# Kernel tuning notes

Measured on AMD Instinct MI355X. Metric: run time of the kernel, lower is better.

Reference implementation:

```python
import jax, jax.numpy as jnp
import numpy as np

N_NODES = 50000
N_EDGES = 800000
D_IN = 64
D_HID = 64
D_OUT = 64


def setup_inputs() -> dict:
    key = jax.random.key(0)
    ks = jax.random.split(key, 10)
    x = jax.random.normal(ks[0], (N_NODES, D_IN), dtype=jnp.float32)
    src = jax.random.randint(ks[1], (N_EDGES,), 0, N_NODES, dtype=jnp.int32)
    dst = jax.random.randint(ks[2], (N_EDGES,), 0, N_NODES, dtype=jnp.int32)
    s = 1.0 / np.sqrt(D_IN)
    W0 = jax.random.uniform(ks[3], (D_IN, D_HID), jnp.float32, -s, s)
    b0 = jnp.zeros((D_HID,), jnp.float32)
    W1 = jax.random.uniform(ks[4], (D_HID, D_HID), jnp.float32, -s, s)
    b1 = jnp.zeros((D_HID,), jnp.float32)
    W2 = jax.random.uniform(ks[5], (D_HID, D_OUT), jnp.float32, -s, s)
    b2 = jnp.zeros((D_OUT,), jnp.float32)
    return {"x": x, "src": src, "dst": dst, "W0": W0, "b0": b0,
            "W1": W1, "b1": b1, "W2": W2, "b2": b2}


def reference(x, src, dst, W0, b0, W1, b1, W2, b2):
    N = x.shape[0]
    # in-degree (constant across layers)
    deg = jax.ops.segment_sum(jnp.ones(src.shape[0], x.dtype), dst, num_segments=N)
    inv = (1.0 / (deg + 1.0))[:, None]  # [N,1] gcn normalizer (deg + self)

    def sage_gcn(h, W, b):
        # gather neighbor feats along edges, scatter-add to destinations
        agg = jax.ops.segment_sum(h[src], dst, num_segments=N)  # [N,d]
        h_neigh = (agg + h) * inv
        return h_neigh @ W + b

    h = sage_gcn(x, W0, b0)
    h = jax.nn.relu(h)
    h = sage_gcn(h, W1, b1)
    h = jax.nn.relu(h)
    h = sage_gcn(h, W2, b2)
    return h
```

## Files before the change

kernel.cpp:

```cpp
#include <hip/hip_runtime.h>
#include <hip/hip_fp16.h>

#define D 64

struct alignas(8) half4v { __half2 a, b; };
typedef _Float16 h2_t __attribute__((ext_vector_type(2)));

union v16u {
    float4 f4;
    h2_t   h2[4];
};

__global__ void count_deg_kernel(const int* __restrict__ dst, int* __restrict__ deg, int nE) {
    int e4 = (blockIdx.x * blockDim.x + threadIdx.x) * 4;
    if (e4 + 3 < nE) {
        int4 d = *(const int4*)(dst + e4);
        atomicAdd(&deg[d.x], 1);
        atomicAdd(&deg[d.y], 1);
        atomicAdd(&deg[d.z], 1);
        atomicAdd(&deg[d.w], 1);
    } else {
        for (int e = e4; e < nE; ++e) atomicAdd(&deg[dst[e]], 1);
    }
}

__global__ __launch_bounds__(256) void scan_a_kernel(const int* __restrict__ deg,
                                                     int* __restrict__ row_ptr,
                                                     int* __restrict__ blocksums, int N) {
    __shared__ int s[256];
    int t = threadIdx.x;
    int i = blockIdx.x * 256 + t;
    int v = (i < N) ? deg[i] : 0;
    s[t] = v;
    __syncthreads();
    #pragma unroll
    for (int d = 1; d < 256; d <<= 1) {
        int u = (t >= d) ? s[t - d] : 0;
        __syncthreads();
        s[t] += u;
        __syncthreads();
    }
    if (i < N) row_ptr[i] = s[t] - v;
    if (t == 255) blocksums[blockIdx.x] = s[255];
}

__global__ __launch_bounds__(256) void scan_b_kernel(int* __restrict__ blocksums,
                                                     int* __restrict__ row_ptr,
                                                     int nb, int N) {
    __shared__ int s[256];
    int t = threadIdx.x;
    int v = (t < nb) ? blocksums[t] : 0;
    s[t] = v;
    __syncthreads();
    #pragma unroll
    for (int d = 1; d < 256; d <<= 1) {
        int u = (t >= d) ? s[t - d] : 0;
        __syncthreads();
        s[t] += u;
        __syncthreads();
    }
    if (t < nb) blocksums[t] = s[t] - v;
    if (t == 255) row_ptr[N] = s[255];
}

__global__ __launch_bounds__(256) void scan_c_kernel(int* __restrict__ row_ptr,
                                                     int* __restrict__ cursor,
                                                     const int* __restrict__ blocksums, int N) {
    int i = blockIdx.x * 256 + threadIdx.x;
    if (i < N) {
        int r = row_ptr[i] + blocksums[blockIdx.x];
        row_ptr[i] = r;
        cursor[i] = r;
    }
}

__global__ __launch_bounds__(256) void fill_csr_sliced_kernel(
    const int* __restrict__ src, const int* __restrict__ dst,
    int* __restrict__ cursor, int* __restrict__ col,
    int nE, int slice_size)
{
    const int g  = blockIdx.x & 7;
    const int gb = blockIdx.x >> 3;
    const int lo = g * slice_size;
    const int hi = lo + slice_size;
    int e4 = (gb * 256 + (int)threadIdx.x) * 4;
    if (e4 + 3 < nE) {
        int4 d = *(const int4*)(dst + e4);
        bool m0 = (d.x >= lo) & (d.x < hi);
        bool m1 = (d.y >= lo) & (d.y < hi);
        bool m2 = (d.z >= lo) & (d.z < hi);
        bool m3 = (d.w >= lo) & (d.w < hi);
        if (m0 | m1 | m2 | m3) {
            int4 s = *(const int4*)(src + e4);
            if (m0) col[atomicAdd(&cursor[d.x], 1)] = s.x;
            if (m1) col[atomicAdd(&cursor[d.y], 1)] = s.y;
            if (m2) col[atomicAdd(&cursor[d.z], 1)] = s.z;
            if (m3) col[atomicAdd(&cursor[d.w], 1)] = s.w;
        }
    } else if (e4 < nE) {
        for (int e = e4; e < nE; ++e) {
            int dd = dst[e];
            if (dd >= lo && dd < hi) col[atomicAdd(&cursor[dd], 1)] = src[e];
        }
    }
}

__global__ __launch_bounds__(256) void cvt_kernel(const float* __restrict__ x,
                                                  __half* __restrict__ xh, int n) {
    int stride = gridDim.x * 256 * 4;
    for (int i = (blockIdx.x * 256 + threadIdx.x) * 4; i + 3 < n; i += stride) {
        float4 v = *(const float4*)(x + i);
        half4v o;
        o.a = __floats2half2_rn(v.x, v.y);
        o.b = __floats2half2_rn(v.z, v.w);
        *(half4v*)(xh + i) = o;
    }
}

__global__ __launch_bounds__(256) void gemm_kernel(
    const __half* __restrict__ hin, const float* __restrict__ W,
    __half* __restrict__ g, int N)
{
    const int j   = threadIdx.x & 63;
    const int wid = (blockIdx.x * blockDim.x + threadIdx.x) >> 6;
    const int nw  = (gridDim.x * blockDim.x) >> 6;

    h2_t wp[32];
    #pragma unroll
    for (int kk = 0; kk < 32; ++kk) {
        h2_t p;
        p[0] = (_Float16)W[(2 * kk + 0) * D + j];
        p[1] = (_Float16)W[(2 * kk + 1) * D + j];
        wp[kk] = p;
    }

    const float4* __restrict__ hin4 = (const float4*)hin;
    for (int r = wid; r < N; r += nw) {
        v16u buf[8];
        #pragma unroll
        for (int t = 0; t < 8; ++t) buf[t].f4 = hin4[(size_t)r * 8 + t];
        float o0 = 0.0f, o1 = 0.0f;
        #pragma unroll
        for (int t = 0; t < 8; ++t) {
            o0 = __builtin_amdgcn_fdot2(buf[t].h2[0], wp[t * 4 + 0], o0, false);
            o1 = __builtin_amdgcn_fdot2(buf[t].h2[1], wp[t * 4 + 1], o1, false);
            o0 = __builtin_amdgcn_fdot2(buf[t].h2[2], wp[t * 4 + 2], o0, false);
            o1 = __builtin_amdgcn_fdot2(buf[t].h2[3], wp[t * 4 + 3], o1, false);
        }
        g[(size_t)r * D + j] = __float2half(o0 + o1);
    }
}

template<bool OUT_H>
__global__ __launch_bounds__(256, 6) void agg_kernel(
    const __half* __restrict__ g, const int* __restrict__ row_ptr,
    const int* __restrict__ col, const float* __restrict__ bias,
    void* __restrict__ hout, int N, int do_relu)
{
    const int lane = threadIdx.x & 63;
    const int sub  = lane >> 4;
    const int fq   = lane & 15;
    const int w    = threadIdx.x >> 6;
    const float4 b4 = ((const float4*)bias)[fq];

    const half4v* __restrict__ gh = (const half4v*)g;

    const int nwaves = gridDim.x * 4;
    for (int i0 = blockIdx.x * 4 + w; i0 < N; i0 += nwaves) {
        const int i   = __builtin_amdgcn_readfirstlane(i0);
        const int rs  = __builtin_amdgcn_readfirstlane(row_ptr[i]);
        const int re  = __builtin_amdgcn_readfirstlane(row_ptr[i + 1]);
        const int deg = re - rs;

        float4 a0 = {0,0,0,0}, a1 = {0,0,0,0}, a2 = {0,0,0,0}, a3 = {0,0,0,0};
        int last_iv = 0;

        for (int e0 = rs; e0 < re; e0 += 64) {
            int ee = e0 + lane;
            int idxv = col[(ee < re) ? ee : (re - 1)];
            last_iv = idxv;
            int rem = re - e0;
            int steps = (((rem < 64) ? rem : 64) + 3) >> 2;
            int t = 0;
            for (; t + 4 <= steps; t += 4) {
                int base = (t << 2) + sub;
                int s0 = __shfl(idxv, base);
                int s1 = __shfl(idxv, base + 4);
                int s2 = __shfl(idxv, base + 8);
                int s3 = __shfl(idxv, base + 12);
                half4v r0 = gh[(size_t)s0 * 16 + fq];
                half4v r1 = gh[(size_t)s1 * 16 + fq];
                half4v r2 = gh[(size_t)s2 * 16 + fq];
                half4v r3 = gh[(size_t)s3 * 16 + fq];
                float2 f;
                f = __half22float2(r0.a); a0.x += f.x; a0.y += f.y;
                f = __half22float2(r0.b); a0.z += f.x; a0.w += f.y;
                f = __half22float2(r1.a); a1.x += f.x; a1.y += f.y;
                f = __half22float2(r1.b); a1.z += f.x; a1.w += f.y;
                f = __half22float2(r2.a); a2.x += f.x; a2.y += f.y;
                f = __half22float2(r2.b); a2.z += f.x; a2.w += f.y;
                f = __half22float2(r3.a); a3.x += f.x; a3.y += f.y;
                f = __half22float2(r3.b); a3.z += f.x; a3.w += f.y;
            }
            for (; t < steps; ++t) {
                int s0 = __shfl(idxv, (t << 2) + sub);
                half4v r0 = gh[(size_t)s0 * 16 + fq];
                float2 f;
                f = __half22float2(r0.a); a0.x += f.x; a0.y += f.y;
                f = __half22float2(r0.b); a0.z += f.x; a0.w += f.y;
            }
        }

        float4 tt;
        tt.x = (a0.x + a1.x) + (a2.x + a3.x);
        tt.y = (a0.y + a1.y) + (a2.y + a3.y);
        tt.z = (a0.z + a1.z) + (a2.z + a3.z);
        tt.w = (a0.w + a1.w) + (a2.w + a3.w);
        tt.x += __shfl_xor(tt.x, 16); tt.x += __shfl_xor(tt.x, 32);
        tt.y += __shfl_xor(tt.y, 16); tt.y += __shfl_xor(tt.y, 32);
        tt.z += __shfl_xor(tt.z, 16); tt.z += __shfl_xor(tt.z, 32);
        tt.w += __shfl_xor(tt.w, 16); tt.w += __shfl_xor(tt.w, 32);

        int pad = (-deg) & 3;
        if (deg > 0 && pad) {
            int last = __shfl(last_iv, 63);
            half4v rl = gh[(size_t)last * 16 + fq];
            float2 f0 = __half22float2(rl.a);
            float2 f1 = __half22float2(rl.b);
            float fp = (float)pad;
            tt.x = fmaf(-fp, f0.x, tt.x);
            tt.y = fmaf(-fp, f0.y, tt.y);
            tt.z = fmaf(-fp, f1.x, tt.z);
            tt.w = fmaf(-fp, f1.y, tt.w);
        }

        half4v rs4 = gh[(size_t)i * 16 + fq];
        float2 s0f = __half22float2(rs4.a);
        float2 s1f = __half22float2(rs4.b);
        float invd = 1.0f / (float)(deg + 1);
        float ox = fmaf(tt.x + s0f.x, invd, b4.x);
        float oy = fmaf(tt.y + s0f.y, invd, b4.y);
        float oz = fmaf(tt.z + s1f.x, invd, b4.z);
        float ow = fmaf(tt.w + s1f.y, invd, b4.w);
        if (do_relu) {
            ox = fmaxf(ox, 0.0f); oy = fmaxf(oy, 0.0f);
            oz = fmaxf(oz, 0.0f); ow = fmaxf(ow, 0.0f);
        }
        if (sub == 0) {
            if constexpr (OUT_H) {
                half4v o;
                o.a = __floats2half2_rn(ox, oy);
                o.b = __floats2half2_rn(oz, ow);
                ((half4v*)hout)[(size_t)i * 16 + fq] = o;
            } else {
                float4 o = make_float4(ox, oy, oz, ow);
                ((float4*)hout)[(size_t)i * 16 + fq] = o;
            }
        }
    }
}

extern "C" void kernel_launch(void* const* d_in, const int* in_sizes, int n_in,
                              void* d_out, int out_size, void* d_ws, size_t ws_size,
                              hipStream_t stream) {
    const float* x   = (const float*)d_in[0];
    const int*   src = (const int*)d_in[1];
    const int*   dst = (const int*)d_in[2];
    const float* W0  = (const float*)d_in[3];
    const float* b0  = (const float*)d_in[4];
    const float* W1  = (const float*)d_in[5];
    const float* b1  = (const float*)d_in[6];
    const float* W2  = (const float*)d_in[7];
    const float* b2  = (const float*)d_in[8];
    float* out = (float*)d_out;

    const int N = in_sizes[0] / D;
    const int E = in_sizes[1];

    const int scan_blocks = (N + 255) / 256;

    char* ws = (char*)d_ws;
    size_t off = 0;
    auto alloc = [&](size_t bytes) -> void* {
        void* p = ws + off;
        off = (off + bytes + 255) & ~(size_t)255;
        return p;
    };
    int*    deg       = (int*)   alloc((size_t)N * sizeof(int));
    int*    row_ptr   = (int*)   alloc((size_t)(N + 1) * sizeof(int));
    int*    cursor    = (int*)   alloc((size_t)N * sizeof(int));
    int*    blocksums = (int*)   alloc((size_t)scan_blocks * sizeof(int));
    int*    col       = (int*)   alloc((size_t)E * sizeof(int));
    __half* xh        = (__half*)alloc((size_t)N * D * sizeof(__half));
    __half* gbuf      = (__half*)alloc((size_t)N * D * sizeof(__half));
    __half* h1        = (__half*)alloc((size_t)N * D * sizeof(__half));
    __half* h2        = (__half*)alloc((size_t)N * D * sizeof(__half));

    hipMemsetAsync(deg, 0, (size_t)N * sizeof(int), stream);
    const int e4_blocks = (E / 4 + 255) / 256;
    count_deg_kernel<<<e4_blocks, 256, 0, stream>>>(dst, deg, E);
    scan_a_kernel<<<scan_blocks, 256, 0, stream>>>(deg, row_ptr, blocksums, N);
    scan_b_kernel<<<1, 256, 0, stream>>>(blocksums, row_ptr, scan_blocks, N);
    scan_c_kernel<<<scan_blocks, 256, 0, stream>>>(row_ptr, cursor, blocksums, N);
    const int slice_size = (N + 7) / 8;
    fill_csr_sliced_kernel<<<e4_blocks * 8, 256, 0, stream>>>(src, dst, cursor, col, E, slice_size);

    cvt_kernel<<<1024, 256, 0, stream>>>(x, xh, N * D);

    const int gemm_blocks = 1024;
    const int agg_blocks  = 4096;

    gemm_kernel<<<gemm_blocks, 256, 0, stream>>>(xh, W0, gbuf, N);
    agg_kernel<true ><<<agg_blocks, 256, 0, stream>>>(gbuf, row_ptr, col, b0, h1,  N, 1);
    gemm_kernel<<<gemm_blocks, 256, 0, stream>>>(h1, W1, gbuf, N);
    agg_kernel<true ><<<agg_blocks, 256, 0, stream>>>(gbuf, row_ptr, col, b1, h2,  N, 1);
    gemm_kernel<<<gemm_blocks, 256, 0, stream>>>(h2, W2, gbuf, N);
    agg_kernel<false><<<agg_blocks, 256, 0, stream>>>(gbuf, row_ptr, col, b2, out, N, 0);
}
```

Measured before the change: 285.4 us.

## Process four nodes per wave in aggregation, one per 16-lane subgroup

Restructures the aggregation kernel so each wavefront handles four destination nodes, one per 16-lane quarter. Each quarter walks its own edge list in chunks of 16 with 16 unrolled gathers and masked accumulation. This removes the cross-subgroup shuffle reduction and the padding correction, and gives better lane use for the low average degree (~16). It costs divergence when degrees differ within a wave and more registers, so launch bounds and grid size are lowered to match.

```diff
diff --git a/kernel.cpp b/kernel.cpp
--- a/kernel.cpp
+++ b/kernel.cpp
@@ -152,7 +152,7 @@
 }
 
 template<bool OUT_H>
-__global__ __launch_bounds__(256, 6) void agg_kernel(
+__global__ __launch_bounds__(256, 4) void agg_kernel(
     const __half* __restrict__ g, const int* __restrict__ row_ptr,
     const int* __restrict__ col, const float* __restrict__ bias,
     void* __restrict__ hout, int N, int do_relu)
@@ -165,49 +165,41 @@
 
     const half4v* __restrict__ gh = (const half4v*)g;
 
-    const int nwaves = gridDim.x * 4;
-    for (int i0 = blockIdx.x * 4 + w; i0 < N; i0 += nwaves) {
-        const int i   = __builtin_amdgcn_readfirstlane(i0);
-        const int rs  = __builtin_amdgcn_readfirstlane(row_ptr[i]);
-        const int re  = __builtin_amdgcn_readfirstlane(row_ptr[i + 1]);
+    const int nwaves  = gridDim.x * 4;
+    const int ngroups = (N + 3) >> 2;
+    for (int grp = blockIdx.x * 4 + w; grp < ngroups; grp += nwaves) {
+        const int node   = grp * 4 + sub;
+        const bool nvalid = node < N;
+        const int ncl = nvalid ? node : (N - 1);
+        const int rs  = row_ptr[ncl];
+        const int re  = nvalid ? row_ptr[ncl + 1] : rs;
         const int deg = re - rs;
 
         float4 a0 = {0,0,0,0}, a1 = {0,0,0,0}, a2 = {0,0,0,0}, a3 = {0,0,0,0};
-        int last_iv = 0;
-
-        for (int e0 = rs; e0 < re; e0 += 64) {
-            int ee = e0 + lane;
-            int idxv = col[(ee < re) ? ee : (re - 1)];
-            last_iv = idxv;
-            int rem = re - e0;
-            int steps = (((rem < 64) ? rem : 64) + 3) >> 2;
-            int t = 0;
-            for (; t + 4 <= steps; t += 4) {
-                int base = (t << 2) + sub;
-                int s0 = __shfl(idxv, base);
-                int s1 = __shfl(idxv, base + 4);
-                int s2 = __shfl(idxv, base + 8);
-                int s3 = __shfl(idxv, base + 12);
-                half4v r0 = gh[(size_t)s0 * 16 + fq];
-                half4v r1 = gh[(size_t)s1 * 16 + fq];
-                half4v r2 = gh[(size_t)s2 * 16 + fq];
-                half4v r3 = gh[(size_t)s3 * 16 + fq];
-                float2 f;
-                f = __half22float2(r0.a); a0.x += f.x; a0.y += f.y;
-                f = __half22float2(r0.b); a0.z += f.x; a0.w += f.y;
-                f = __half22float2(r1.a); a1.x += f.x; a1.y += f.y;
-                f = __half22float2(r1.b); a1.z += f.x; a1.w += f.y;
-                f = __half22float2(r2.a); a2.x += f.x; a2.y += f.y;
-                f = __half22float2(r2.b); a2.z += f.x; a2.w += f.y;
-                f = __half22float2(r3.a); a3.x += f.x; a3.y += f.y;
-                f = __half22float2(r3.b); a3.z += f.x; a3.w += f.y;
+
+        for (int e0 = rs; ; e0 += 16) {
+            if (__ballot(e0 < re) == 0ULL) break;
+            int ee = e0 + fq;
+            int cl = (ee < re) ? ee : ((re > rs) ? re - 1 : 0);
+            int idxv = col[cl];
+
+            half4v rr[16];
+            #pragma unroll
+            for (int r = 0; r < 16; ++r) {
+                int s = __shfl(idxv, (sub << 4) + r);
+                rr[r] = gh[(size_t)s * 16 + fq];
             }
-            for (; t < steps; ++t) {
-                int s0 = __shfl(idxv, (t << 2) + sub);
-                half4v r0 = gh[(size_t)s0 * 16 + fq];
-                float2 f;
-                f = __half22float2(r0.a); a0.x += f.x; a0.y += f.y;
-                f = __half22float2(r0.b); a0.z += f.x; a0.w += f.y;
+            #pragma unroll
+            for (int r = 0; r < 16; ++r) {
+                float m = (e0 + r < re) ? 1.0f : 0.0f;
+                float2 f0 = __half22float2(rr[r].a);
+                float2 f1 = __half22float2(rr[r].b);
+                float4& a = (r & 3) == 0 ? a0 : (r & 3) == 1 ? a1
+                          : (r & 3) == 2 ? a2 : a3;
+                a.x = fmaf(m, f0.x, a.x);
+                a.y = fmaf(m, f0.y, a.y);
+                a.z = fmaf(m, f1.x, a.z);
+                a.w = fmaf(m, f1.y, a.w);
             }
         }
 
@@ -216,27 +208,10 @@
         tt.y = (a0.y + a1.y) + (a2.y + a3.y);
         tt.z = (a0.z + a1.z) + (a2.z + a3.z);
         tt.w = (a0.w + a1.w) + (a2.w + a3.w);
-        tt.x += __shfl_xor(tt.x, 16); tt.x += __shfl_xor(tt.x, 32);
-        tt.y += __shfl_xor(tt.y, 16); tt.y += __shfl_xor(tt.y, 32);
-        tt.z += __shfl_xor(tt.z, 16); tt.z += __shfl_xor(tt.z, 32);
-        tt.w += __shfl_xor(tt.w, 16); tt.w += __shfl_xor(tt.w, 32);
-
-        int pad = (-deg) & 3;
-        if (deg > 0 && pad) {
-            int last = __shfl(last_iv, 63);
-            half4v rl = gh[(size_t)last * 16 + fq];
-            float2 f0 = __half22float2(rl.a);
-            float2 f1 = __half22float2(rl.b);
-            float fp = (float)pad;
-            tt.x = fmaf(-fp, f0.x, tt.x);
-            tt.y = fmaf(-fp, f0.y, tt.y);
-            tt.z = fmaf(-fp, f1.x, tt.z);
-            tt.w = fmaf(-fp, f1.y, tt.w);
-        }
-
-        half4v rs4 = gh[(size_t)i * 16 + fq];
-        float2 s0f = __half22float2(rs4.a);
-        float2 s1f = __half22float2(rs4.b);
+
+        half4v sv = gh[(size_t)ncl * 16 + fq];
+        float2 s0f = __half22float2(sv.a);
+        float2 s1f = __half22float2(sv.b);
         float invd = 1.0f / (float)(deg + 1);
         float ox = fmaf(tt.x + s0f.x, invd, b4.x);
         float oy = fmaf(tt.y + s0f.y, invd, b4.y);
@@ -246,15 +221,14 @@
             ox = fmaxf(ox, 0.0f); oy = fmaxf(oy, 0.0f);
             oz = fmaxf(oz, 0.0f); ow = fmaxf(ow, 0.0f);
         }
-        if (sub == 0) {
+        if (nvalid) {
             if constexpr (OUT_H) {
                 half4v o;
                 o.a = __floats2half2_rn(ox, oy);
                 o.b = __floats2half2_rn(oz, ow);
-                ((half4v*)hout)[(size_t)i * 16 + fq] = o;
+                ((half4v*)hout)[(size_t)node * 16 + fq] = o;
             } else {
-                float4 o = make_float4(ox, oy, oz, ow);
-                ((float4*)hout)[(size_t)i * 16 + fq] = o;
+                ((float4*)hout)[(size_t)node * 16 + fq] = make_float4(ox, oy, oz, ow);
             }
         }
     }
@@ -308,7 +282,7 @@
     cvt_kernel<<<1024, 256, 0, stream>>>(x, xh, N * D);
 
     const int gemm_blocks = 1024;
-    const int agg_blocks  = 4096;
+    const int agg_blocks  = 3136;
 
     gemm_kernel<<<gemm_blocks, 256, 0, stream>>>(xh, W0, gbuf, N);
     agg_kernel<true ><<<agg_blocks, 256, 0, stream>>>(gbuf, row_ptr, col, b0, h1,  N, 1);
```

Result: no change. 284.0 us (-0.5%).
